# Kernel tuning notes

Measured on AMD Instinct MI355X. Metric: run time of the kernel, lower is better.

The kernel has to match this reference:

```python
import jax, jax.numpy as jnp
from jax import lax
import numpy as np

L, G, C = 4, 2, 4  # num_blocks, num_sparsity_groups, num_sparsity_cardinals
IMAGE_MEAN = 0.5
SCALE = 2


def _wn(v, g):
    # weight_norm over dims (1,2,3), g per output channel
    n = jnp.sqrt(jnp.sum(v * v, axis=(1, 2, 3), keepdims=True))
    return (g.reshape(-1, 1, 1, 1) / n) * v


def _conv(x, w, b, pad):
    y = lax.conv_general_dilated(x, w, (1, 1), [(pad, pad), (pad, pad)],
                                 dimension_numbers=('NCHW', 'OIHW', 'NCHW'))
    return y + b[None, :, None, None]


def _dyn_conv(x, v, g, b, mw, mb):
    # sparsity-routed conv: per-sample expert mixture of kernels
    w = _wn(v, g)                                   # [G*out, in, k, k]
    B = x.shape[0]
    logits = x.mean((-1, -2)) @ mw.T + mb           # [B, G*C]
    s = jax.nn.softmax(logits.reshape(B, G, C), axis=1)
    wv = w.reshape(G, C, -1, *w.shape[1:])          # [G, C, D, in, k, k]
    wper = jnp.einsum('bgc,gcdikl->bcdikl', s, wv)
    wper = wper.reshape(B, -1, *w.shape[1:])        # [B, out, in, k, k]
    bper = jnp.einsum('bgc,gcd->bcd', s, b.reshape(G, C, -1)).reshape(B, -1)

    def per_sample(xi, wi, bi):
        yi = lax.conv_general_dilated(xi[None], wi, (1, 1), [(1, 1), (1, 1)],
                                      dimension_numbers=('NCHW', 'OIHW', 'NCHW'))[0]
        return yi + bi[:, None, None]

    return jax.vmap(per_sample)(x, wper, bper)


def _pixel_shuffle(x, r):
    B, Cc, H, W = x.shape
    x = x.reshape(B, Cc // (r * r), r, r, H, W)
    x = x.transpose(0, 1, 4, 2, 5, 3)
    return x.reshape(B, Cc // (r * r), H * r, W * r)


def setup_inputs() -> dict:
    key = jax.random.key(0)
    ks = jax.random.split(key, 16)
    f32 = jnp.float32
    inp = {
        'x': jax.random.uniform(ks[0], (8, 3, 64, 64), dtype=f32),
        'head_v': jax.random.normal(ks[1], (64, 3, 3, 3), dtype=f32) * 0.05,
        'head_g': jnp.ones((64,), f32),
        'head_b': jnp.zeros((64,), f32),
        'b1_v': jax.random.normal(ks[2], (L, 512, 64, 3, 3), dtype=f32) * 0.05,
        'b1_g': jnp.full((L, 512), 2.0, f32),
        'b1_b': jnp.zeros((L, 512), f32),
        'b1_mw': jax.random.normal(ks[3], (L, 8, 64), dtype=f32) * 0.05,
        'b1_mb': jax.random.normal(ks[4], (L, 8), dtype=f32) * 0.05,
        'b2_v': jax.random.normal(ks[5], (L, 128, 256, 3, 3), dtype=f32) * 0.05,
        'b2_g': jnp.full((L, 128), 1.0 / np.sqrt(L), f32),
        'b2_b': jnp.zeros((L, 128), f32),
        'b2_mw': jax.random.normal(ks[6], (L, 8, 256), dtype=f32) * 0.05,
        'b2_mb': jax.random.normal(ks[7], (L, 8), dtype=f32) * 0.05,
        'tail_v': jax.random.normal(ks[8], (12, 64, 3, 3), dtype=f32) * 0.05,
        'tail_g': jnp.ones((12,), f32),
        'tail_b': jnp.zeros((12,), f32),
        'skip_v': jax.random.normal(ks[9], (12, 3, 5, 5), dtype=f32) * 0.05,
        'skip_g': jnp.ones((12,), f32),
        'skip_b': jnp.zeros((12,), f32),
    }
    return inp


def reference(x, head_v, head_g, head_b,
              b1_v, b1_g, b1_b, b1_mw, b1_mb,
              b2_v, b2_g, b2_b, b2_mw, b2_mb,
              tail_v, tail_g, tail_b,
              skip_v, skip_g, skip_b):
    x = x - IMAGE_MEAN
    h = _conv(x, _wn(head_v, head_g), head_b, pad=1)
    for l in range(L):
        r0 = h
        t = _dyn_conv(h, b1_v[l], b1_g[l], b1_b[l], b1_mw[l], b1_mb[l])
        t = jax.nn.relu(t)
        t = _dyn_conv(t, b2_v[l], b2_g[l], b2_b[l], b2_mw[l], b2_mb[l])
        h = t + r0
    body = _conv(h, _wn(tail_v, tail_g), tail_b, pad=1)
    s = _conv(x, _wn(skip_v, skip_g), skip_b, pad=2)
    y = _pixel_shuffle(body + s, SCALE) + IMAGE_MEAN
    return y
```

## Files before the change

### kernel.cpp

```cpp
#include <hip/hip_runtime.h>

typedef __attribute__((ext_vector_type(8))) short bf16x8;
typedef __attribute__((ext_vector_type(4))) float f32x4;
typedef __attribute__((ext_vector_type(8))) unsigned short u16x8;

__device__ __forceinline__ unsigned short bf16u(float x) {
    unsigned int u = __builtin_bit_cast(unsigned int, x);
    unsigned int r = (u + 0x7fffu + ((u >> 16) & 1u)) >> 16;
    return (unsigned short)r;
}
__device__ __forceinline__ float bf2f(unsigned short u) {
    return __builtin_bit_cast(float, (unsigned int)u << 16);
}
__device__ __forceinline__ void gll16(const void* g, void* l) {
    __builtin_amdgcn_global_load_lds((const __attribute__((address_space(1))) void*)g,
                                     (__attribute__((address_space(3))) void*)l, 16, 0, 0);
}

__global__ __launch_bounds__(256) void zero_all(unsigned short* __restrict__ hbf,
                                                unsigned short* __restrict__ tbf,
                                                float* __restrict__ sums) {
    int i = blockIdx.x * 256 + threadIdx.x;
    u16x8 z8 = {0, 0, 0, 0, 0, 0, 0, 0};
    if (i < 16640) {
        int chv = i & 3, pb = i >> 2, pos = pb % 260, bc = pb / 260;
        int y, x;
        if (pos < 66) { y = 0; x = pos; }
        else if (pos < 132) { y = 65; x = pos - 66; }
        else if (pos < 196) { y = pos - 131; x = 0; }
        else { y = pos - 195; x = 65; }
        *(u16x8*)&hbf[((size_t)bc * 4356 + y * 66 + x) * 32 + chv * 8] = z8;
    } else if (i < 83200) {
        int j = i - 16640;
        int chv = j & 3, pb = j >> 2, pos = pb % 260, bc = pb / 260;
        int y, x;
        if (pos < 66) { y = 0; x = pos; }
        else if (pos < 132) { y = 65; x = pos - 66; }
        else if (pos < 196) { y = pos - 131; x = 0; }
        else { y = pos - 195; x = 65; }
        *(u16x8*)&tbf[((size_t)bc * 4356 + y * 66 + x) * 32 + chv * 8] = z8;
    } else {
        int k = i - 83200;
        f32x4 z4 = {0.f, 0.f, 0.f, 0.f};
        ((f32x4*)sums)[k] = z4;
    }
}

__global__ __launch_bounds__(256) void wn_all(
    const float* __restrict__ hv, const float* __restrict__ hg, float* __restrict__ hw,
    const float* __restrict__ tv, const float* __restrict__ tg, float* __restrict__ tw,
    const float* __restrict__ kv, const float* __restrict__ kg, float* __restrict__ kw,
    const float* __restrict__ b1v, const float* __restrict__ b1g, float* __restrict__ b1s,
    const float* __restrict__ b2v, const float* __restrict__ b2g, float* __restrict__ b2s) {
    int blk = blockIdx.x;
    const float *v, *g;
    float *outw = nullptr, *outs = nullptr;
    int len, row;
    if (blk < 64)        { v = hv;  g = hg;  outw = hw;  len = 27;   row = blk; }
    else if (blk < 76)   { v = tv;  g = tg;  outw = tw;  len = 576;  row = blk - 64; }
    else if (blk < 88)   { v = kv;  g = kg;  outw = kw;  len = 75;   row = blk - 76; }
    else if (blk < 2136) { v = b1v; g = b1g; outs = b1s; len = 576;  row = blk - 88; }
    else                 { v = b2v; g = b2g; outs = b2s; len = 2304; row = blk - 2136; }

    __shared__ float red[4];
    __shared__ float s_sc;
    const float* vr = v + (size_t)row * len;
    float ss = 0.f;
    for (int i = threadIdx.x; i < len; i += 256) { float a = vr[i]; ss += a * a; }
    for (int o = 32; o > 0; o >>= 1) ss += __shfl_down(ss, o);
    if ((threadIdx.x & 63) == 0) red[threadIdx.x >> 6] = ss;
    __syncthreads();
    if (threadIdx.x == 0) s_sc = g[row] / sqrtf(red[0] + red[1] + red[2] + red[3]);
    __syncthreads();
    float sc = s_sc;
    if (outs) {
        if (threadIdx.x == 0) outs[row] = sc;
    } else {
        float* orow = outw + (size_t)row * len;
        for (int i = threadIdx.x; i < len; i += 256) orow[i] = vr[i] * sc;
    }
}

template <int IC, int GOC, int LGG, int LGMO>
__global__ __launch_bounds__(256) void combine_v2(
    const float* __restrict__ v, const float* __restrict__ scale,
    const float* __restrict__ msum, const float* __restrict__ mw,
    const float* __restrict__ mb, float* __restrict__ s_out,
    unsigned short* __restrict__ wq, int D, int OC) {
    constexpr int ROWF = IC * 9;
    constexpr int KCh = IC / 32;
    constexpr int TOTC = GOC * KCh * 9 * 4;
    __shared__ float lv[2 * GOC * ROWF];
    __shared__ float lg[8], sv8[8];
    int tid = threadIdx.x;
    int b = blockIdx.y, ocg = blockIdx.x * GOC;
    {
        int j = tid >> 5, l32 = tid & 31;
        float part = 0.f;
        for (int i = l32; i < IC; i += 32) part += msum[b * IC + i] * mw[j * IC + i];
        for (int m = 16; m > 0; m >>= 1) part += __shfl_xor(part, m);
        if (l32 == 0) lg[j] = part * (1.f / 4096.f) + mb[j];
    }
    for (int i = tid; i < 2 * GOC * ROWF; i += 256) {
        int r = i / ROWF, jj = i - r * ROWF;
        int oc_r = (r / GOC) * OC + ocg + (r % GOC);
        lv[i] = v[(size_t)oc_r * ROWF + jj] * scale[oc_r];
    }
    __syncthreads();
    if (tid < 8) {
        int g = tid >> 2, c = tid & 3;
        float l0 = lg[c], l1 = lg[4 + c];
        float m = fmaxf(l0, l1);
        float e0 = __expf(l0 - m), e1 = __expf(l1 - m);
        float val = ((g == 0) ? e0 : e1) / (e0 + e1);
        sv8[tid] = val;
        if (blockIdx.x == 0) s_out[b * 8 + tid] = val;
    }
    __syncthreads();
    for (int ci = tid; ci < TOTC; ci += 256) {
        int ml = ci & (GOC - 1);
        int c = ci >> LGG;
        int kg = c & 3, c2 = c >> 2;
        int t = c2 % 9, kc = c2 / 9;
        int oc = ocg + ml;
        int cd = oc / D;
        float s0 = sv8[cd], s1 = sv8[4 + cd];
        const float* p0 = &lv[(size_t)ml * ROWF];
        const float* p1 = &lv[(size_t)(GOC + ml) * ROWF];
        u16x8 pk;
#pragma unroll
        for (int kj = 0; kj < 8; ++kj) {
            int ic9 = (kc * 32 + kg * 8 + kj) * 9 + t;
            pk[kj] = bf16u(s0 * p0[ic9] + s1 * p1[ic9]);
        }
        size_t w_off = ((((size_t)(b * (OC >> LGMO) + (oc >> LGMO)) * KCh + kc) * 9 + t) * 4 + kg)
                           * ((1 << LGMO) * 8) + (size_t)(oc & ((1 << LGMO) - 1)) * 8;
        *(u16x8*)&wq[w_off] = pk;
    }
}

__global__ void tail_repack(const float* __restrict__ tw, unsigned short* __restrict__ wq) {
    int idx = blockIdx.x * 256 + threadIdx.x;
    int kj = idx & 7;
    int tmp = idx >> 3;
    int mo = tmp % 16; tmp /= 16;
    int kg = tmp & 3; tmp >>= 2;
    int t = tmp % 9; tmp /= 9;
    int kc = tmp;
    int ic = kc * 32 + kg * 8 + kj;
    float val = (mo < 12) ? tw[((size_t)mo * 64 + ic) * 9 + t] : 0.f;
    wq[idx] = bf16u(val);
}

template <int IC, int OC, int MT, int WM, int WN, int NR,
          bool RELU, bool RES, bool WF32, bool WBF, int OCR, bool DYNB, int MINW>
__global__ __launch_bounds__(WM * WN * 64, MINW)
void conv_mfma(
    const unsigned short* __restrict__ in_bf,
    const unsigned short* __restrict__ wq,
    const float* __restrict__ bias_raw, const float* __restrict__ s8, int lgD,
    float* __restrict__ out,
    unsigned short* __restrict__ out_bf, float* __restrict__ msum, long wstride) {
    constexpr int THREADS = WM * WN * 64;
    constexpr int KCH = IC / 32;
    constexpr int NRH = NR + 2;
    constexpr int NT = NR * 64;
    constexpr int NF = (NT / 16) / WN;
    constexpr int MW = MT / (16 * WM);
    constexpr int WELEM = 9 * 32 * MT;
    constexpr int SELEM = NRH * 66 * 32;
    constexpr int SCH = SELEM / 8;
    constexpr int OCB = OCR / 32;

    __shared__ __align__(16) unsigned short S[2][SELEM];
    __shared__ float MRED[WN][MT];

    const int b = blockIdx.y, ot = blockIdx.z;
    const int y0 = blockIdx.x * NR;
    const int tid = threadIdx.x;
    const int lane = tid & 63;
    const int wid = tid >> 6;
    const int wm = wid / WN, wn = wid % WN;
    const int l15 = lane & 15, lk = lane >> 4;
    const int wmo = wm * (MT / WM);
    const int wno = wn * (NT / WN);

    f32x4 acc[MW][NF];
#pragma unroll
    for (int mf = 0; mf < MW; ++mf)
#pragma unroll
        for (int nf = 0; nf < NF; ++nf)
#pragma unroll
            for (int q = 0; q < 4; ++q) acc[mf][nf][q] = 0.f;

    const unsigned short* inb = in_bf + (size_t)b * KCH * (4356 * 32);
    const unsigned short* wqb = wq + (size_t)b * wstride + (size_t)ot * (KCH * WELEM);
    const unsigned short* wqa = wqb + (size_t)lk * (MT * 8) + (size_t)(wmo + l15) * 8;

    auto STAGE_S = [&](int kc, int buf) {
        const unsigned short* sb = inb + (size_t)kc * (4356 * 32);
        for (int i = tid; i < SCH; i += THREADS) {
            int Lz = i ^ ((i >> 3) & 7);
            int lk2 = Lz & 3, cr = Lz >> 2;
            int col = cr % 66, row = cr / 66;
            gll16(sb + ((size_t)(y0 + row) * 66 + col) * 32 + lk2 * 8,
                  (char*)S[buf] + i * 16);
        }
    };

    STAGE_S(0, 0);
    __syncthreads();
    for (int kc = 0; kc < KCH; ++kc) {
        if (kc + 1 < KCH) STAGE_S(kc + 1, (kc + 1) & 1);
        const unsigned short* Sb = S[kc & 1];
        const unsigned short* wk = wqa + (size_t)kc * WELEM;
        bf16x8 aN[MW];
#pragma unroll
        for (int mf = 0; mf < MW; ++mf)
            aN[mf] = *(const bf16x8*)(wk + mf * (16 * 8));
#pragma unroll
        for (int t = 0; t < 9; ++t) {
            const int dy = t / 3, dx = t % 3;
            bf16x8 aC[MW];
#pragma unroll
            for (int mf = 0; mf < MW; ++mf) aC[mf] = aN[mf];
            if (t < 8) {
#pragma unroll
                for (int mf = 0; mf < MW; ++mf)
                    aN[mf] = *(const bf16x8*)(wk + (t + 1) * (4 * MT * 8) + mf * (16 * 8));
            }
#pragma unroll
            for (int nf = 0; nf < NF; ++nf) {
                int n = wno + nf * 16 + l15;
                int r = n >> 6, c = n & 63;
                int L = ((r + dy) * 66 + (c + dx)) * 4 + lk;
                int P = L ^ ((L >> 3) & 7);
                bf16x8 bv = *(const bf16x8*)((const char*)Sb + P * 16);
#pragma unroll
                for (int mf = 0; mf < MW; ++mf)
                    acc[mf][nf] = __builtin_amdgcn_mfma_f32_16x16x32_bf16(aC[mf], bv, acc[mf][nf], 0, 0, 0);
            }
        }
        __syncthreads();
    }

    if constexpr (WBF) {
        static_assert(NF == 2, "shuffle epilogue needs NF==2");
        const int mynf = lk & 1;
        const int ch = lk >> 1;
        const bool evenlk = ((lk & 1) == 0);
#pragma unroll
        for (int mf = 0; mf < MW; ++mf) {
            int ocb = ot * MT + wmo + mf * 16 + lk * 4;
            float bvv[4];
#pragma unroll
            for (int q = 0; q < 4; ++q) {
                int oc = ocb + q;
                if (DYNB) {
                    int cc = oc >> lgD;
                    bvv[q] = s8[b * 8 + cc] * bias_raw[oc] + s8[b * 8 + 4 + cc] * bias_raw[OCR + oc];
                } else {
                    bvv[q] = bias_raw[oc];
                }
            }
            float r[2][4], pr[2][4];
#pragma unroll
            for (int nf = 0; nf < 2; ++nf)
#pragma unroll
                for (int q = 0; q < 4; ++q) {
                    float v = acc[mf][nf][q] + bvv[q];
                    if (RELU) v = fmaxf(v, 0.f);
                    r[nf][q] = v;
                }
#pragma unroll
            for (int nf = 0; nf < 2; ++nf)
#pragma unroll
                for (int q = 0; q < 4; ++q) pr[nf][q] = __shfl_xor(r[nf][q], 16);
            float v8[8];
#pragma unroll
            for (int q = 0; q < 4; ++q) {
                float a = r[mynf][q], p = pr[mynf][q];
                v8[q] = evenlk ? a : p;
                v8[4 + q] = evenlk ? p : a;
            }
            int n = wno + mynf * 16 + l15;
            int y = y0 + (n >> 6), x = n & 63;
            int occ = ot * MT + wmo + mf * 16 + ch * 8;
            size_t addr = ((((size_t)b * OCB + (occ >> 5)) * 66 + (y + 1)) * 66 + (x + 1)) * 32
                          + (occ & 31);
            if (RES) {
                u16x8 rv = *(const u16x8*)&out_bf[addr];
#pragma unroll
                for (int j = 0; j < 8; ++j) v8[j] += bf2f(rv[j]);
            }
            u16x8 pk;
#pragma unroll
            for (int j = 0; j < 8; ++j) pk[j] = bf16u(v8[j]);
            *(u16x8*)&out_bf[addr] = pk;
            if (msum) {
#pragma unroll
                for (int j = 0; j < 8; ++j) {
                    float t = v8[j];
                    t += __shfl_xor(t, 1);
                    t += __shfl_xor(t, 2);
                    t += __shfl_xor(t, 4);
                    t += __shfl_xor(t, 8);
                    t += __shfl_xor(t, 16);
                    v8[j] = t;
                }
                if ((lane & 31) == 0) {
#pragma unroll
                    for (int j = 0; j < 8; ++j)
                        MRED[wn][wmo + mf * 16 + ch * 8 + j] = v8[j];
                }
            }
        }
        if (msum) {
            __syncthreads();
            if (tid < MT) {
                float tot = 0.f;
#pragma unroll
                for (int w2 = 0; w2 < WN; ++w2) tot += MRED[w2][tid];
                atomicAdd(&msum[b * OCR + ot * MT + tid], tot);
            }
        }
    }
    if constexpr (WF32) {
#pragma unroll
        for (int mf = 0; mf < MW; ++mf) {
            int ocb = ot * MT + wmo + mf * 16 + lk * 4;
#pragma unroll
            for (int nf = 0; nf < NF; ++nf) {
                int n = wno + nf * 16 + l15;
                int y = y0 + (n >> 6), x = n & 63;
#pragma unroll
                for (int q = 0; q < 4; ++q) {
                    int oc = ocb + q;
                    if (oc < OCR) {
                        float v = acc[mf][nf][q] + bias_raw[oc];
                        out[(((size_t)b * OCR + oc) * 64 + y) * 64 + x] = v;
                    }
                }
            }
        }
    }
}

__global__ __launch_bounds__(256) void head_conv(
    const float* __restrict__ in, const float* __restrict__ w,
    const float* __restrict__ bias,
    unsigned short* __restrict__ out_bf, float* __restrict__ hsum0) {
    constexpr int OCT = 16, IC = 3;
    __shared__ float s_in[34 * 34];
    __shared__ float s_w[OCT * 9];
    __shared__ float wred[4][OCT];
    int b = blockIdx.z;
    int ocBase = blockIdx.y * OCT;
    int ty0 = (blockIdx.x >> 1) * 32;
    int tx0 = (blockIdx.x & 1) * 32;
    int tid = threadIdx.x;
    int lane = tid & 63, wid = tid >> 6;
    int tx = tid & 15, ty = tid >> 4;

    float acc[OCT][4];
#pragma unroll
    for (int oc = 0; oc < OCT; ++oc)
#pragma unroll
        for (int p = 0; p < 4; ++p) acc[oc][p] = 0.f;

    const float* inb = in + (size_t)b * IC * 4096;
    for (int ic = 0; ic < IC; ++ic) {
        const float* src = inb + (size_t)ic * 4096;
        for (int i = tid; i < 34 * 34; i += 256) {
            int r = i / 34, cc = i % 34;
            int gy = ty0 + r - 1, gx = tx0 + cc - 1;
            float val = 0.f;
            if (gy >= 0 && gy < 64 && gx >= 0 && gx < 64) val = src[gy * 64 + gx] - 0.5f;
            s_in[i] = val;
        }
        for (int i = tid; i < OCT * 9; i += 256) {
            int oc = i / 9, t = i % 9;
            s_w[i] = w[((size_t)(ocBase + oc) * IC + ic) * 9 + t];
        }
        __syncthreads();
        float v[4][4];
#pragma unroll
        for (int r = 0; r < 4; ++r)
#pragma unroll
            for (int cc = 0; cc < 4; ++cc) v[r][cc] = s_in[(2 * ty + r) * 34 + (2 * tx + cc)];
#pragma unroll
        for (int oc = 0; oc < OCT; ++oc) {
#pragma unroll
            for (int ky = 0; ky < 3; ++ky)
#pragma unroll
                for (int kx = 0; kx < 3; ++kx) {
                    float wv = s_w[oc * 9 + ky * 3 + kx];
                    acc[oc][0] += wv * v[ky][kx];
                    acc[oc][1] += wv * v[ky][kx + 1];
                    acc[oc][2] += wv * v[ky + 1][kx];
                    acc[oc][3] += wv * v[ky + 1][kx + 1];
                }
        }
        __syncthreads();
    }
    int py = ty0 + 2 * ty, px = tx0 + 2 * tx;
#pragma unroll
    for (int oc = 0; oc < OCT; ++oc) {
        int og = ocBase + oc;
        float bv = bias[og];
        float osum = 0.f;
#pragma unroll
        for (int p = 0; p < 4; ++p) {
            int dy = p >> 1, dx = p & 1;
            float val = acc[oc][p] + bv;
            osum += val;
            out_bf[((size_t)(b * 2 + (og >> 5)) * 4356 + (py + dy + 1) * 66 + (px + dx + 1)) * 32
                   + (og & 31)] = bf16u(val);
        }
        for (int m = 1; m < 64; m <<= 1) osum += __shfl_xor(osum, m);
        if (lane == 0) wred[wid][oc] = osum;
    }
    __syncthreads();
    if (tid < OCT)
        atomicAdd(&hsum0[b * 64 + ocBase + tid],
                  wred[0][tid] + wred[1][tid] + wred[2][tid] + wred[3][tid]);
}

__global__ __launch_bounds__(256) void shuffle_skip(
    const float* __restrict__ body, const float* __restrict__ x,
    const float* __restrict__ skw, const float* __restrict__ skb,
    float* __restrict__ out) {
    __shared__ float w[900];
    __shared__ float bb[12];
    int tid = threadIdx.x;
    for (int i = tid; i < 900; i += 256) w[i] = skw[i];
    if (tid < 12) bb[tid] = skb[tid];
    __syncthreads();
    int idx = blockIdx.x * 256 + tid;
    int ox = idx & 127;
    int oy = (idx >> 7) & 127;
    int v = idx >> 14;
    int c = v % 3;
    int b = v / 3;
    int rx = ox & 1, ry = oy & 1;
    int xx = ox >> 1, yy = oy >> 1;
    int ch = c * 4 + ry * 2 + rx;
    float acc = bb[ch];
    for (int ic = 0; ic < 3; ++ic)
        for (int ky = 0; ky < 5; ++ky) {
            int gy = yy + ky - 2;
            if (gy < 0 || gy >= 64) continue;
            for (int kx = 0; kx < 5; ++kx) {
                int gx = xx + kx - 2;
                if (gx < 0 || gx >= 64) continue;
                acc += w[((ch * 3 + ic) * 5 + ky) * 5 + kx] *
                       (x[((size_t)(b * 3 + ic) * 64 + gy) * 64 + gx] - 0.5f);
            }
        }
    size_t src = (((size_t)b * 12 + ch) * 64 + yy) * 64 + xx;
    out[idx] = body[src] + acc + 0.5f;
}

extern "C" void kernel_launch(void* const* d_in, const int* in_sizes, int n_in,
                              void* d_out, int out_size, void* d_ws, size_t ws_size,
                              hipStream_t stream) {
    const float* x      = (const float*)d_in[0];
    const float* head_v = (const float*)d_in[1];
    const float* head_g = (const float*)d_in[2];
    const float* head_b = (const float*)d_in[3];
    const float* b1_v   = (const float*)d_in[4];
    const float* b1_g   = (const float*)d_in[5];
    const float* b1_b   = (const float*)d_in[6];
    const float* b1_mw  = (const float*)d_in[7];
    const float* b1_mb  = (const float*)d_in[8];
    const float* b2_v   = (const float*)d_in[9];
    const float* b2_g   = (const float*)d_in[10];
    const float* b2_b   = (const float*)d_in[11];
    const float* b2_mw  = (const float*)d_in[12];
    const float* b2_mb  = (const float*)d_in[13];
    const float* tail_v = (const float*)d_in[14];
    const float* tail_g = (const float*)d_in[15];
    const float* tail_b = (const float*)d_in[16];
    const float* skip_v = (const float*)d_in[17];
    const float* skip_g = (const float*)d_in[18];
    const float* skip_b = (const float*)d_in[19];

    float* ws = (float*)d_ws;
    size_t off = 0;
    auto alloc = [&](size_t n) { float* p = ws + off; off += (n + 3) & ~(size_t)3; return p; };
    float* head_w = alloc(64 * 27);
    float* tail_w = alloc(12 * 576);
    float* skip_w = alloc(12 * 75);
    float* b1_sc  = alloc(2048);
    float* b2_sc  = alloc(512);
    float* sums   = alloc(10240);
    float* sbuf   = alloc(64);
    float* body   = alloc((size_t)8 * 12 * 4096);
    unsigned short* wq1  = (unsigned short*)alloc((size_t)8 * 256 * 576 / 2);
    unsigned short* wq2  = (unsigned short*)alloc((size_t)8 * 64 * 2304 / 2);
    unsigned short* wqt  = (unsigned short*)alloc(9216 / 2);
    unsigned short* h_bf = (unsigned short*)alloc((size_t)8 * 2 * 4356 * 32 / 2);
    unsigned short* t_bf = (unsigned short*)alloc((size_t)8 * 8 * 4356 * 32 / 2);
    (void)ws_size; (void)in_sizes; (void)n_in; (void)out_size;

    auto hsum = [&](int l) { return sums + l * 512; };
    auto tsum = [&](int l) { return sums + 2048 + l * 2048; };

    zero_all<<<335, 256, 0, stream>>>(h_bf, t_bf, sums);
    wn_all<<<2648, 256, 0, stream>>>(head_v, head_g, head_w, tail_v, tail_g, tail_w,
                                     skip_v, skip_g, skip_w, b1_v, b1_g, b1_sc,
                                     b2_v, b2_g, b2_sc);
    head_conv<<<dim3(4, 4, 8), 256, 0, stream>>>(x, head_w, head_b, h_bf, hsum(0));
    tail_repack<<<36, 256, 0, stream>>>(tail_w, wqt);

    for (int l = 0; l < 4; ++l) {
        combine_v2<64, 4, 2, 5><<<dim3(64, 8), 256, 0, stream>>>(
            b1_v + (size_t)l * 512 * 576, b1_sc + (size_t)l * 512, hsum(l),
            b1_mw + (size_t)l * 8 * 64, b1_mb + l * 8, sbuf, wq1, 64, 256);
        conv_mfma<64, 256, 32, 1, 4, 2, true, false, false, true, 256, true, 4>
            <<<dim3(32, 8, 8), 256, 0, stream>>>(h_bf, wq1, b1_b + (size_t)l * 512, sbuf, 6,
                                                 nullptr, t_bf, tsum(l), 147456);
        combine_v2<256, 2, 1, 6><<<dim3(32, 8), 256, 0, stream>>>(
            b2_v + (size_t)l * 128 * 2304, b2_sc + (size_t)l * 128, tsum(l),
            b2_mw + (size_t)l * 8 * 256, b2_mb + l * 8, sbuf, wq2, 16, 64);
        conv_mfma<256, 64, 64, 2, 4, 2, false, true, false, true, 64, true, 2>
            <<<dim3(32, 8, 1), 512, 0, stream>>>(t_bf, wq2, b2_b + (size_t)l * 128, sbuf, 4,
                                                 nullptr, h_bf, (l < 3) ? hsum(l + 1) : nullptr,
                                                 147456);
    }

    conv_mfma<64, 16, 16, 1, 4, 4, false, false, true, false, 12, false, 2>
        <<<dim3(16, 8, 1), 256, 0, stream>>>(h_bf, wqt, tail_b, nullptr, 0,
                                             body, nullptr, nullptr, 0);
    shuffle_skip<<<1536, 256, 0, stream>>>(body, x, skip_w, skip_b, (float*)d_out);
}
```

Before: 336.8 us.

## Fuse weight-norm into combine kernels, batch samples per block, retile conv2

Merges the zeroing and weight-norm setup kernels into one launch and folds the tail weight-norm into its repack kernel. The big per-block weight-norm scales are now computed inside the combine kernels, which also handle four samples per block so each expert weight row is loaded once per four samples instead of once per sample. The MFMA conv switches to a two-slot register double buffer for weight fragments across the flattened kc/tap loop. The block index mapping swaps batch and row so neighbouring blocks hit the same weight slice, and the second conv is retiled to 4x2 warps with a single row per block and higher occupancy. Together these cut launches and redundant global weight reads, at the cost of more register pressure and more serial per-block work in the combine kernels.

```diff
diff --git a/kernel.cpp b/kernel.cpp
--- a/kernel.cpp
+++ b/kernel.cpp
@@ -17,51 +17,45 @@
                                      (__attribute__((address_space(3))) void*)l, 16, 0, 0);
 }
 
-__global__ __launch_bounds__(256) void zero_all(unsigned short* __restrict__ hbf,
-                                                unsigned short* __restrict__ tbf,
-                                                float* __restrict__ sums) {
-    int i = blockIdx.x * 256 + threadIdx.x;
-    u16x8 z8 = {0, 0, 0, 0, 0, 0, 0, 0};
-    if (i < 16640) {
-        int chv = i & 3, pb = i >> 2, pos = pb % 260, bc = pb / 260;
-        int y, x;
-        if (pos < 66) { y = 0; x = pos; }
-        else if (pos < 132) { y = 65; x = pos - 66; }
-        else if (pos < 196) { y = pos - 131; x = 0; }
-        else { y = pos - 195; x = 65; }
-        *(u16x8*)&hbf[((size_t)bc * 4356 + y * 66 + x) * 32 + chv * 8] = z8;
-    } else if (i < 83200) {
-        int j = i - 16640;
-        int chv = j & 3, pb = j >> 2, pos = pb % 260, bc = pb / 260;
-        int y, x;
-        if (pos < 66) { y = 0; x = pos; }
-        else if (pos < 132) { y = 65; x = pos - 66; }
-        else if (pos < 196) { y = pos - 131; x = 0; }
-        else { y = pos - 195; x = 65; }
-        *(u16x8*)&tbf[((size_t)bc * 4356 + y * 66 + x) * 32 + chv * 8] = z8;
-    } else {
-        int k = i - 83200;
-        f32x4 z4 = {0.f, 0.f, 0.f, 0.f};
-        ((f32x4*)sums)[k] = z4;
-    }
-}
-
-__global__ __launch_bounds__(256) void wn_all(
+__global__ __launch_bounds__(256) void setup_kernel(
+    unsigned short* __restrict__ hbf, unsigned short* __restrict__ tbf,
+    float* __restrict__ sums,
     const float* __restrict__ hv, const float* __restrict__ hg, float* __restrict__ hw,
-    const float* __restrict__ tv, const float* __restrict__ tg, float* __restrict__ tw,
-    const float* __restrict__ kv, const float* __restrict__ kg, float* __restrict__ kw,
-    const float* __restrict__ b1v, const float* __restrict__ b1g, float* __restrict__ b1s,
-    const float* __restrict__ b2v, const float* __restrict__ b2g, float* __restrict__ b2s) {
+    const float* __restrict__ kv, const float* __restrict__ kg, float* __restrict__ kw) {
     int blk = blockIdx.x;
+    if (blk < 335) {
+        int i = blk * 256 + threadIdx.x;
+        u16x8 z8 = {0, 0, 0, 0, 0, 0, 0, 0};
+        if (i < 16640) {
+            int chv = i & 3, pb = i >> 2, pos = pb % 260, bc = pb / 260;
+            int y, x;
+            if (pos < 66) { y = 0; x = pos; }
+            else if (pos < 132) { y = 65; x = pos - 66; }
+            else if (pos < 196) { y = pos - 131; x = 0; }
+            else { y = pos - 195; x = 65; }
+            *(u16x8*)&hbf[((size_t)bc * 4356 + y * 66 + x) * 32 + chv * 8] = z8;
+        } else if (i < 83200) {
+            int j = i - 16640;
+            int chv = j & 3, pb = j >> 2, pos = pb % 260, bc = pb / 260;
+            int y, x;
+            if (pos < 66) { y = 0; x = pos; }
+            else if (pos < 132) { y = 65; x = pos - 66; }
+            else if (pos < 196) { y = pos - 131; x = 0; }
+            else { y = pos - 195; x = 65; }
+            *(u16x8*)&tbf[((size_t)bc * 4356 + y * 66 + x) * 32 + chv * 8] = z8;
+        } else {
+            int k = i - 83200;
+            f32x4 z4 = {0.f, 0.f, 0.f, 0.f};
+            ((f32x4*)sums)[k] = z4;
+        }
+        return;
+    }
+    int b2 = blk - 335;
     const float *v, *g;
-    float *outw = nullptr, *outs = nullptr;
+    float* outw;
     int len, row;
-    if (blk < 64)        { v = hv;  g = hg;  outw = hw;  len = 27;   row = blk; }
-    else if (blk < 76)   { v = tv;  g = tg;  outw = tw;  len = 576;  row = blk - 64; }
-    else if (blk < 88)   { v = kv;  g = kg;  outw = kw;  len = 75;   row = blk - 76; }
-    else if (blk < 2136) { v = b1v; g = b1g; outs = b1s; len = 576;  row = blk - 88; }
-    else                 { v = b2v; g = b2g; outs = b2s; len = 2304; row = blk - 2136; }
-
+    if (b2 < 64) { v = hv; g = hg; outw = hw; len = 27; row = b2; }
+    else         { v = kv; g = kg; outw = kw; len = 75; row = b2 - 64; }
     __shared__ float red[4];
     __shared__ float s_sc;
     const float* vr = v + (size_t)row * len;
@@ -73,83 +67,140 @@
     if (threadIdx.x == 0) s_sc = g[row] / sqrtf(red[0] + red[1] + red[2] + red[3]);
     __syncthreads();
     float sc = s_sc;
-    if (outs) {
-        if (threadIdx.x == 0) outs[row] = sc;
+    float* orow = outw + (size_t)row * len;
+    for (int i = threadIdx.x; i < len; i += 256) orow[i] = vr[i] * sc;
+}
+
+__global__ __launch_bounds__(256) void tail_repack2(const float* __restrict__ tv,
+                                                    const float* __restrict__ tg,
+                                                    unsigned short* __restrict__ wq) {
+    __shared__ float row[576];
+    __shared__ float red[4];
+    __shared__ float s_sc;
+    int mo = blockIdx.x;
+    int tid = threadIdx.x;
+    if (mo < 12) {
+        for (int i = tid; i < 576; i += 256) row[i] = tv[mo * 576 + i];
+        __syncthreads();
+        float ss = 0.f;
+        for (int i = tid; i < 576; i += 256) { float a = row[i]; ss += a * a; }
+        for (int o = 32; o > 0; o >>= 1) ss += __shfl_down(ss, o);
+        if ((tid & 63) == 0) red[tid >> 6] = ss;
+        __syncthreads();
+        if (tid == 0) s_sc = tg[mo] / sqrtf(red[0] + red[1] + red[2] + red[3]);
+        __syncthreads();
+        float sc = s_sc;
+        for (int ch = tid; ch < 72; ch += 256) {
+            int kg = ch & 3, c2 = ch >> 2;
+            int t = c2 % 9, kc = c2 / 9;
+            u16x8 pk;
+#pragma unroll
+            for (int kj = 0; kj < 8; ++kj) {
+                int ic = kc * 32 + kg * 8 + kj;
+                pk[kj] = bf16u(row[ic * 9 + t] * sc);
+            }
+            *(u16x8*)&wq[(size_t)((kc * 9 + t) * 4 + kg) * 128 + mo * 8] = pk;
+        }
     } else {
-        float* orow = outw + (size_t)row * len;
-        for (int i = threadIdx.x; i < len; i += 256) orow[i] = vr[i] * sc;
-    }
-}
-
-template <int IC, int GOC, int LGG, int LGMO>
-__global__ __launch_bounds__(256) void combine_v2(
-    const float* __restrict__ v, const float* __restrict__ scale,
+        u16x8 z = {0, 0, 0, 0, 0, 0, 0, 0};
+        for (int ch = tid; ch < 72; ch += 256) {
+            int kg = ch & 3, c2 = ch >> 2;
+            int t = c2 % 9, kc = c2 / 9;
+            *(u16x8*)&wq[(size_t)((kc * 9 + t) * 4 + kg) * 128 + mo * 8] = z;
+        }
+    }
+}
+
+template <int IC, int GOC, int BPB, int LGMO>
+__global__ __launch_bounds__(256) void combine_v3(
+    const float* __restrict__ v, const float* __restrict__ g,
     const float* __restrict__ msum, const float* __restrict__ mw,
     const float* __restrict__ mb, float* __restrict__ s_out,
     unsigned short* __restrict__ wq, int D, int OC) {
     constexpr int ROWF = IC * 9;
     constexpr int KCh = IC / 32;
+    constexpr int ROWS2 = 2 * GOC;
     constexpr int TOTC = GOC * KCh * 9 * 4;
-    __shared__ float lv[2 * GOC * ROWF];
-    __shared__ float lg[8], sv8[8];
+    __shared__ float lv[ROWS2 * ROWF];
+    __shared__ float lg[BPB][8];
+    __shared__ float sv[BPB][8];
+    __shared__ float scr[ROWS2];
+    __shared__ float sw[BPB][ROWS2];
     int tid = threadIdx.x;
-    int b = blockIdx.y, ocg = blockIdx.x * GOC;
+    int ocg = blockIdx.x * GOC;
+    int b0 = blockIdx.y * BPB;
+    for (int i = tid; i < ROWS2 * ROWF; i += 256) {
+        int r = i / ROWF, jj = i - r * ROWF;
+        int oc_r = (r / GOC) * OC + ocg + (r % GOC);
+        lv[i] = v[(size_t)oc_r * ROWF + jj];
+    }
     {
         int j = tid >> 5, l32 = tid & 31;
-        float part = 0.f;
-        for (int i = l32; i < IC; i += 32) part += msum[b * IC + i] * mw[j * IC + i];
-        for (int m = 16; m > 0; m >>= 1) part += __shfl_xor(part, m);
-        if (l32 == 0) lg[j] = part * (1.f / 4096.f) + mb[j];
-    }
-    for (int i = tid; i < 2 * GOC * ROWF; i += 256) {
-        int r = i / ROWF, jj = i - r * ROWF;
-        int oc_r = (r / GOC) * OC + ocg + (r % GOC);
-        lv[i] = v[(size_t)oc_r * ROWF + jj] * scale[oc_r];
-    }
-    __syncthreads();
-    if (tid < 8) {
-        int g = tid >> 2, c = tid & 3;
-        float l0 = lg[c], l1 = lg[4 + c];
+        for (int bb = 0; bb < BPB; ++bb) {
+            float part = 0.f;
+            for (int i = l32; i < IC; i += 32) part += msum[(b0 + bb) * IC + i] * mw[j * IC + i];
+            for (int m = 16; m > 0; m >>= 1) part += __shfl_xor(part, m);
+            if (l32 == 0) lg[bb][j] = part * (1.f / 4096.f) + mb[j];
+        }
+    }
+    __syncthreads();
+    {
+        constexpr int TPR = 256 / ROWS2;
+        int r = tid / TPR, lr = tid % TPR;
+        float ss = 0.f;
+        for (int i = lr; i < ROWF; i += TPR) { float a = lv[r * ROWF + i]; ss += a * a; }
+#pragma unroll
+        for (int m = (TPR > 32 ? 32 : TPR / 2); m > 0; m >>= 1) ss += __shfl_xor(ss, m);
+        if (lr == 0) {
+            int oc_r = (r / GOC) * OC + ocg + (r % GOC);
+            scr[r] = g[oc_r] / sqrtf(ss);
+        }
+    }
+    if (tid < BPB * 8) {
+        int bb = tid >> 3, j = tid & 7;
+        int gg = j >> 2, c = j & 3;
+        float l0 = lg[bb][c], l1 = lg[bb][4 + c];
         float m = fmaxf(l0, l1);
         float e0 = __expf(l0 - m), e1 = __expf(l1 - m);
-        float val = ((g == 0) ? e0 : e1) / (e0 + e1);
-        sv8[tid] = val;
-        if (blockIdx.x == 0) s_out[b * 8 + tid] = val;
+        float val = ((gg == 0) ? e0 : e1) / (e0 + e1);
+        sv[bb][j] = val;
+        if (blockIdx.x == 0) s_out[(b0 + bb) * 8 + j] = val;
+    }
+    __syncthreads();
+    if (tid < BPB * ROWS2) {
+        int bb = tid / ROWS2, r = tid % ROWS2;
+        int oc = ocg + (r % GOC);
+        int cd = oc / D;
+        float s = (r < GOC) ? sv[bb][cd] : sv[bb][4 + cd];
+        sw[bb][r] = s * scr[r];
     }
     __syncthreads();
     for (int ci = tid; ci < TOTC; ci += 256) {
-        int ml = ci & (GOC - 1);
-        int c = ci >> LGG;
+        int ml = ci % GOC;
+        int c = ci / GOC;
         int kg = c & 3, c2 = c >> 2;
         int t = c2 % 9, kc = c2 / 9;
         int oc = ocg + ml;
-        int cd = oc / D;
-        float s0 = sv8[cd], s1 = sv8[4 + cd];
         const float* p0 = &lv[(size_t)ml * ROWF];
         const float* p1 = &lv[(size_t)(GOC + ml) * ROWF];
-        u16x8 pk;
+        float a0[8], a1[8];
 #pragma unroll
         for (int kj = 0; kj < 8; ++kj) {
             int ic9 = (kc * 32 + kg * 8 + kj) * 9 + t;
-            pk[kj] = bf16u(s0 * p0[ic9] + s1 * p1[ic9]);
-        }
-        size_t w_off = ((((size_t)(b * (OC >> LGMO) + (oc >> LGMO)) * KCh + kc) * 9 + t) * 4 + kg)
-                           * ((1 << LGMO) * 8) + (size_t)(oc & ((1 << LGMO) - 1)) * 8;
-        *(u16x8*)&wq[w_off] = pk;
-    }
-}
-
-__global__ void tail_repack(const float* __restrict__ tw, unsigned short* __restrict__ wq) {
-    int idx = blockIdx.x * 256 + threadIdx.x;
-    int kj = idx & 7;
-    int tmp = idx >> 3;
-    int mo = tmp % 16; tmp /= 16;
-    int kg = tmp & 3; tmp >>= 2;
-    int t = tmp % 9; tmp /= 9;
-    int kc = tmp;
-    int ic = kc * 32 + kg * 8 + kj;
-    float val = (mo < 12) ? tw[((size_t)mo * 64 + ic) * 9 + t] : 0.f;
-    wq[idx] = bf16u(val);
+            a0[kj] = p0[ic9];
+            a1[kj] = p1[ic9];
+        }
+        for (int bb = 0; bb < BPB; ++bb) {
+            float s0 = sw[bb][ml], s1 = sw[bb][GOC + ml];
+            u16x8 pk;
+#pragma unroll
+            for (int kj = 0; kj < 8; ++kj) pk[kj] = bf16u(s0 * a0[kj] + s1 * a1[kj]);
+            int b = b0 + bb;
+            size_t w_off = ((((size_t)(b * (OC >> LGMO) + (oc >> LGMO)) * KCh + kc) * 9 + t) * 4 + kg)
+                               * ((1 << LGMO) * 8) + (size_t)(oc & ((1 << LGMO) - 1)) * 8;
+            *(u16x8*)&wq[w_off] = pk;
+        }
+    }
 }
 
 template <int IC, int OC, int MT, int WM, int WN, int NR,
@@ -175,8 +226,8 @@
     __shared__ __align__(16) unsigned short S[2][SELEM];
     __shared__ float MRED[WN][MT];
 
-    const int b = blockIdx.y, ot = blockIdx.z;
-    const int y0 = blockIdx.x * NR;
+    const int b = blockIdx.x, ot = blockIdx.z;
+    const int y0 = blockIdx.y * NR;
     const int tid = threadIdx.x;
     const int lane = tid & 63;
     const int wid = tid >> 6;
@@ -208,27 +259,23 @@
         }
     };
 
+    bf16x8 aT[2][MW];
+#pragma unroll
+    for (int mf = 0; mf < MW; ++mf) {
+        aT[0][mf] = *(const bf16x8*)(wqa + mf * 128);
+        aT[1][mf] = *(const bf16x8*)(wqa + (4 * MT * 8) + mf * 128);
+    }
     STAGE_S(0, 0);
     __syncthreads();
+#pragma unroll
     for (int kc = 0; kc < KCH; ++kc) {
         if (kc + 1 < KCH) STAGE_S(kc + 1, (kc + 1) & 1);
         const unsigned short* Sb = S[kc & 1];
-        const unsigned short* wk = wqa + (size_t)kc * WELEM;
-        bf16x8 aN[MW];
-#pragma unroll
-        for (int mf = 0; mf < MW; ++mf)
-            aN[mf] = *(const bf16x8*)(wk + mf * (16 * 8));
 #pragma unroll
         for (int t = 0; t < 9; ++t) {
+            const int gt = kc * 9 + t;
+            const int pp = gt & 1;
             const int dy = t / 3, dx = t % 3;
-            bf16x8 aC[MW];
-#pragma unroll
-            for (int mf = 0; mf < MW; ++mf) aC[mf] = aN[mf];
-            if (t < 8) {
-#pragma unroll
-                for (int mf = 0; mf < MW; ++mf)
-                    aN[mf] = *(const bf16x8*)(wk + (t + 1) * (4 * MT * 8) + mf * (16 * 8));
-            }
 #pragma unroll
             for (int nf = 0; nf < NF; ++nf) {
                 int n = wno + nf * 16 + l15;
@@ -238,7 +285,14 @@
                 bf16x8 bv = *(const bf16x8*)((const char*)Sb + P * 16);
 #pragma unroll
                 for (int mf = 0; mf < MW; ++mf)
-                    acc[mf][nf] = __builtin_amdgcn_mfma_f32_16x16x32_bf16(aC[mf], bv, acc[mf][nf], 0, 0, 0);
+                    acc[mf][nf] = __builtin_amdgcn_mfma_f32_16x16x32_bf16(aT[pp][mf], bv, acc[mf][nf], 0, 0, 0);
+            }
+            if (gt + 2 < KCH * 9) {
+                const int ngt = gt + 2;
+                const int nkc = ngt / 9, nt2 = ngt % 9;
+#pragma unroll
+                for (int mf = 0; mf < MW; ++mf)
+                    aT[pp][mf] = *(const bf16x8*)(wqa + (size_t)nkc * WELEM + nt2 * (4 * MT * 8) + mf * 128);
             }
         }
         __syncthreads();
@@ -489,10 +543,7 @@
     size_t off = 0;
     auto alloc = [&](size_t n) { float* p = ws + off; off += (n + 3) & ~(size_t)3; return p; };
     float* head_w = alloc(64 * 27);
-    float* tail_w = alloc(12 * 576);
     float* skip_w = alloc(12 * 75);
-    float* b1_sc  = alloc(2048);
-    float* b2_sc  = alloc(512);
     float* sums   = alloc(10240);
     float* sbuf   = alloc(64);
     float* body   = alloc((size_t)8 * 12 * 4096);
@@ -506,31 +557,29 @@
     auto hsum = [&](int l) { return sums + l * 512; };
     auto tsum = [&](int l) { return sums + 2048 + l * 2048; };
 
-    zero_all<<<335, 256, 0, stream>>>(h_bf, t_bf, sums);
-    wn_all<<<2648, 256, 0, stream>>>(head_v, head_g, head_w, tail_v, tail_g, tail_w,
-                                     skip_v, skip_g, skip_w, b1_v, b1_g, b1_sc,
-                                     b2_v, b2_g, b2_sc);
+    setup_kernel<<<411, 256, 0, stream>>>(h_bf, t_bf, sums, head_v, head_g, head_w,
+                                          skip_v, skip_g, skip_w);
+    tail_repack2<<<16, 256, 0, stream>>>(tail_v, tail_g, wqt);
     head_conv<<<dim3(4, 4, 8), 256, 0, stream>>>(x, head_w, head_b, h_bf, hsum(0));
-    tail_repack<<<36, 256, 0, stream>>>(tail_w, wqt);
 
     for (int l = 0; l < 4; ++l) {
-        combine_v2<64, 4, 2, 5><<<dim3(64, 8), 256, 0, stream>>>(
-            b1_v + (size_t)l * 512 * 576, b1_sc + (size_t)l * 512, hsum(l),
+        combine_v3<64, 4, 4, 5><<<dim3(64, 2), 256, 0, stream>>>(
+            b1_v + (size_t)l * 512 * 576, b1_g + (size_t)l * 512, hsum(l),
             b1_mw + (size_t)l * 8 * 64, b1_mb + l * 8, sbuf, wq1, 64, 256);
         conv_mfma<64, 256, 32, 1, 4, 2, true, false, false, true, 256, true, 4>
-            <<<dim3(32, 8, 8), 256, 0, stream>>>(h_bf, wq1, b1_b + (size_t)l * 512, sbuf, 6,
+            <<<dim3(8, 32, 8), 256, 0, stream>>>(h_bf, wq1, b1_b + (size_t)l * 512, sbuf, 6,
                                                  nullptr, t_bf, tsum(l), 147456);
-        combine_v2<256, 2, 1, 6><<<dim3(32, 8), 256, 0, stream>>>(
-            b2_v + (size_t)l * 128 * 2304, b2_sc + (size_t)l * 128, tsum(l),
+        combine_v3<256, 2, 4, 6><<<dim3(32, 2), 256, 0, stream>>>(
+            b2_v + (size_t)l * 128 * 2304, b2_g + (size_t)l * 128, tsum(l),
             b2_mw + (size_t)l * 8 * 256, b2_mb + l * 8, sbuf, wq2, 16, 64);
-        conv_mfma<256, 64, 64, 2, 4, 2, false, true, false, true, 64, true, 2>
-            <<<dim3(32, 8, 1), 512, 0, stream>>>(t_bf, wq2, b2_b + (size_t)l * 128, sbuf, 4,
+        conv_mfma<256, 64, 64, 4, 2, 1, false, true, false, true, 64, true, 4>
+            <<<dim3(8, 64, 1), 512, 0, stream>>>(t_bf, wq2, b2_b + (size_t)l * 128, sbuf, 4,
                                                  nullptr, h_bf, (l < 3) ? hsum(l + 1) : nullptr,
                                                  147456);
     }
 
     conv_mfma<64, 16, 16, 1, 4, 4, false, false, true, false, 12, false, 2>
-        <<<dim3(16, 8, 1), 256, 0, stream>>>(h_bf, wqt, tail_b, nullptr, 0,
+        <<<dim3(8, 16, 1), 256, 0, stream>>>(h_bf, wqt, tail_b, nullptr, 0,
                                              body, nullptr, nullptr, 0);
     shuffle_skip<<<1536, 256, 0, stream>>>(body, x, skip_w, skip_b, (float*)d_out);
 }
```

Result: no change. 338.1 us (+0.4%).
